# Kernel optimization log

Hardware: AMD Instinct MI355X
Metric: run time of the kernel (lower is better)

Reference implementation:

```python
import jax, jax.numpy as jnp
import numpy as np
from jax import lax

NUM_INPUT = 4
NUM_OUTPUT = 1
NUM_U = 10
N = NUM_U // NUM_OUTPUT          # MPC horizon
BATCH = 1024
NINEQ_U = 2 * NUM_U              # input box constraints
NINEQ_X = 2 * NUM_INPUT * N      # soft state constraints
NZ = NUM_U                       # control decision variable dim
NE = NINEQ_X                     # slack variable dim
NW = NZ + NE                     # combined QP variable w = [z; e]
IPM_ITERS = 20                   # fixed-iteration primal-dual interior point
SIGMA = 0.1                      # centering parameter
REG = 1e-8                       # KKT regularization


def setup_inputs():
    key = jax.random.key(0)
    ks = jax.random.split(key, 6)
    x = 0.5 * jax.random.normal(ks[0], (BATCH, NUM_INPUT), dtype=jnp.float32)
    # equality constraint pins z0 = u0; keep inside the |z| <= 0.5 box so QP is feasible
    u0 = (jax.random.uniform(ks[1], (BATCH, NUM_OUTPUT), dtype=jnp.float32) - 0.5) * 0.8
    Q_sqrt = jax.random.uniform(ks[2], (NUM_INPUT, NUM_INPUT), dtype=jnp.float32)
    R_sqrt = jax.random.uniform(ks[3], (NUM_OUTPUT, NUM_OUTPUT), dtype=jnp.float32)
    # scale A so that A^N stays bounded (torch init rand() would blow up at N=10)
    A_dyn = 0.3 * jax.random.uniform(ks[4], (NUM_INPUT, NUM_INPUT), dtype=jnp.float32)
    B_dyn = jax.random.uniform(ks[5], (NUM_INPUT, NUM_OUTPUT), dtype=jnp.float32)
    return {"x": x, "u0": u0, "Q_sqrt": Q_sqrt, "R_sqrt": R_sqrt,
            "A_dyn": A_dyn, "B_dyn": B_dyn}


def _build_mpc_blocks(A, B):
    # A_hat = [A; A^2; ...; A^N],  B_hat = lower block-Toeplitz of A^k B
    Apows = [A]
    for _ in range(1, N):
        Apows.append(Apows[-1] @ A)
    A_hat = jnp.concatenate(Apows, axis=0)                 # (N*n, n)
    T = [B]
    for _ in range(1, N):
        T.append(A @ T[-1])
    T = jnp.stack(T)                                        # (N, n, m), T[k] = A^k B
    i = jnp.arange(N)
    diff = i[:, None] - i[None, :]
    blocks = jnp.where((diff >= 0)[:, :, None, None],
                       T[jnp.clip(diff, 0, N - 1)], 0.0)    # (N, N, n, m)
    B_hat = blocks.transpose(0, 2, 1, 3).reshape(N * NUM_INPUT, N * NUM_OUTPUT)
    return A_hat, B_hat


def _max_step(v, dv):
    # largest alpha keeping v + alpha*dv > 0 (per batch row)
    ratio = jnp.where(dv < -1e-12, -v / jnp.minimum(dv, -1e-12), 1e8)
    return jnp.min(ratio, axis=-1, keepdims=True)


def _qp_solve(H, q, G, h, Aeq, beq):
    # min 0.5 w^T H w + q^T w  s.t. G w <= h, Aeq w = beq
    # H, G, Aeq shared; q, h, beq batched. Infeasible-start primal-dual IPM.
    b, nw = q.shape
    mI = G.shape[0]
    ne = Aeq.shape[0]
    w = jnp.zeros((b, nw), q.dtype)
    nu = jnp.zeros((b, ne), q.dtype)
    s = jnp.maximum(h, 1.0)
    lam = jnp.ones((b, mI), q.dtype)
    I_nw = jnp.eye(nw, dtype=q.dtype)
    I_ne = jnp.eye(ne, dtype=q.dtype)

    def step(carry, _):
        w, s, lam, nu = carry
        Gw = w @ G.T
        r_dual = w @ H + q + lam @ G + nu @ Aeq            # (b, nw)
        r_prim = Gw + s - h                                # (b, mI)
        r_eq = w @ Aeq.T - beq                             # (b, ne)
        mu = SIGMA * jnp.sum(s * lam, axis=-1, keepdims=True) / mI
        d = lam / s
        tmp = (mu - lam * s + lam * r_prim) / s
        rw = -(r_dual + tmp @ G)
        rn = -r_eq
        # Schur complement in w: M = H + G^T diag(lam/s) G
        M = H[None] + (G.T[None, :, :] * d[:, None, :]) @ G + REG * I_nw
        AeqT = jnp.broadcast_to(Aeq.T[None], (b, nw, ne))
        AeqB = jnp.broadcast_to(Aeq[None], (b, ne, nw))
        corner = jnp.broadcast_to((-REG * I_ne)[None], (b, ne, ne))
        K = jnp.concatenate([jnp.concatenate([M, AeqT], axis=2),
                             jnp.concatenate([AeqB, corner], axis=2)], axis=1)
        rhs = jnp.concatenate([rw, rn], axis=1)
        sol = jnp.linalg.solve(K, rhs[..., None])[..., 0]
        dw, dnu = sol[:, :nw], sol[:, nw:]
        ds = -(dw @ G.T) - r_prim
        dlam = (mu - lam * s - lam * ds) / s
        alpha = 0.99 * jnp.minimum(1.0, jnp.minimum(_max_step(s, ds),
                                                    _max_step(lam, dlam)))
        return (w + alpha * dw, s + alpha * ds,
                lam + alpha * dlam, nu + alpha * dnu), None

    (w, s, lam, nu), _ = lax.scan(step, (w, s, lam, nu), None, length=IPM_ITERS)
    return w


def _forward(x, u0, Q_sqrt, R_sqrt, A_dyn, B_dyn):
    b = x.shape[0]
    dt = x.dtype
    x0 = x.reshape(b, -1)
    A_hat, B_hat = _build_mpc_blocks(A_dyn, B_dyn)
    Q = Q_sqrt @ Q_sqrt.T
    R = R_sqrt @ R_sqrt.T
    Q_diag = jnp.kron(jnp.eye(N, dtype=dt), Q)   # block-diag(Q,...,Q,P) with P = Q
    R_diag = jnp.kron(jnp.eye(N, dtype=dt), R)
    Q_hat = B_hat.T @ (Q_diag @ B_hat) + R_diag  # (nz, nz)
    A_x0 = x0 @ A_hat.T                           # (b, n*N)
    p = 2.0 * A_x0 @ (Q_diag @ B_hat)             # (b, nz)
    G1 = jnp.concatenate([jnp.eye(NZ, dtype=dt), -jnp.eye(NZ, dtype=dt)], axis=0)
    G2 = jnp.concatenate([B_hat, -B_hat], axis=0)
    h1 = 0.5 * jnp.ones((b, NINEQ_U), dt)
    h21 = 4.0 * jnp.ones((b, NUM_INPUT * N), dt) - A_x0
    h22 = 4.0 * jnp.ones((b, NUM_INPUT * N), dt) + A_x0
    h2 = jnp.concatenate([h21, h22], axis=1)
    E = jnp.eye(NE, dtype=dt)                     # E_sqrt = I so E = I
    # combined QP over w = [z; e]:
    #   min z^T Q_hat z + p^T z + e^T E e
    #   s.t. G1 z <= h1, G2 z - e <= h2, -e <= 0, F z = f
    # (sum_squares(sqrtm(Q_hat) z) == z^T Q_hat z, so sqrtm cancels exactly)
    H = 2.0 * jnp.block([[Q_hat, jnp.zeros((NZ, NE), dt)],
                         [jnp.zeros((NE, NZ), dt), E]])
    q = jnp.concatenate([p, jnp.zeros((b, NE), dt)], axis=1)
    Ie = jnp.eye(NE, dtype=dt)
    G_all = jnp.concatenate([
        jnp.concatenate([G1, jnp.zeros((NINEQ_U, NE), dt)], axis=1),
        jnp.concatenate([G2, -Ie], axis=1),
        jnp.concatenate([jnp.zeros((NE, NZ), dt), -Ie], axis=1)], axis=0)
    h_all = jnp.concatenate([h1, h2, jnp.zeros((b, NE), dt)], axis=1)
    F = jnp.zeros((1, NW), dt).at[0, 0].set(1.0)  # F z = f with F = e_0^T (padded over e)
    beq = u0.reshape(b, -1)
    w = _qp_solve(H, q, G_all, h_all, F, beq)
    u_opt = w[:, :NZ]
    e_opt = w[:, NZ:]
    a = jnp.sum((u_opt @ Q_hat) * u_opt + p * u_opt, axis=1)
    bterm = jnp.sum((A_x0 @ Q_diag) * A_x0, axis=1)
    c = jnp.sum((x0 @ Q) * x0, axis=1)
    dterm = jnp.sum((e_opt @ E) * e_opt, axis=1)
    cost_opt = (a + bterm + c + dterm)[:, None]
    u0_opt = u_opt[:, 0]   # weight vector is e_0
    return cost_opt, u0_opt


def reference(x, u0, Q_sqrt, R_sqrt, A_dyn, B_dyn):
    return _forward(x, u0, Q_sqrt, R_sqrt, A_dyn, B_dyn)
```

## Files before the change

kernel.cpp:

```cpp
#include <hip/hip_runtime.h>

#define BATCH 1024
#define ITERS 20
#define SIGMA_C 0.1f
#define REG_C 1e-8f

typedef float f2 __attribute__((ext_vector_type(2)));

__device__ __forceinline__ float frcp(float x) { return __builtin_amdgcn_rcpf(x); }
__device__ __forceinline__ float readlane_f(float v, int l) {
    return __int_as_float(__builtin_amdgcn_readlane(__float_as_int(v), l));
}
__device__ __forceinline__ f2 mkf2(float a, float b) { f2 r; r.x = a; r.y = b; return r; }
__device__ __forceinline__ f2 fma2(f2 a, f2 b, f2 c) { return a * b + c; }

#define DPPF(v, ctrl) \
    __int_as_float(__builtin_amdgcn_update_dpp(0, __float_as_int(v), ctrl, 0xf, 0xf, true))

__device__ __forceinline__ float wave_sum(float v) {
    v += DPPF(v, 0xB1);
    v += DPPF(v, 0x4E);
    v += DPPF(v, 0x141);
    v += DPPF(v, 0x140);
    v += __shfl_xor(v, 16);
    v += __shfl_xor(v, 32);
    return v;
}

#define RED4_DPP(ctrl) do { \
    p0 += DPPF(p0, ctrl); \
    p1 += DPPF(p1, ctrl); \
    p2 += DPPF(p2, ctrl); \
    q = fmaxf(q, DPPF(q, ctrl)); \
} while (0)

__global__ __launch_bounds__(64, 1) void ipm_kernel(
    const float* __restrict__ x, const float* __restrict__ u0p,
    const float* __restrict__ Qs, const float* __restrict__ Rs,
    const float* __restrict__ Ad, const float* __restrict__ Bd,
    float* __restrict__ out)
{
    const int item = blockIdx.x;
    const int lane = threadIdx.x;

    __shared__ __align__(16) float BLc[10 * 40];
    __shared__ __align__(16) float QBc[10 * 40];
    __shared__ __align__(16) float yL4[40];
    __shared__ __align__(16) float QhL[10 * 12];
    __shared__ __align__(16) float SL[10 * 12];
    __shared__ __align__(16) float cg[80];
    __shared__ float duL[20], ltL[20];
    __shared__ float axL[40];
    __shared__ float pvL[10], wL[10];
    __shared__ float QL[16];
    __shared__ float TL[40];
    __shared__ float AhL[160];

    const int r2 = (lane >> 2) & 3, c2 = lane & 3;
    const int r4 = lane & 3;

    if (lane < 16) {
        float acc = 0.f;
        #pragma unroll
        for (int k = 0; k < 4; ++k) acc += Qs[r2 * 4 + k] * Qs[c2 * 4 + k];
        QL[lane] = acc;
    }

    float acol[4];
    #pragma unroll
    for (int k = 0; k < 4; ++k) acol[k] = Ad[k * 4 + c2];
    float cur = Ad[r2 * 4 + c2];
    if (lane < 16) AhL[r2 * 4 + c2] = cur;
    #pragma unroll
    for (int i = 1; i < 10; ++i) {
        float nx = 0.f;
        #pragma unroll
        for (int k = 0; k < 4; ++k) nx += __shfl(cur, r2 * 4 + k) * acol[k];
        cur = nx;
        if (lane < 16) AhL[(4 * i + r2) * 4 + c2] = cur;
    }

    float arow[4];
    #pragma unroll
    for (int k = 0; k < 4; ++k) arow[k] = Ad[r4 * 4 + k];
    float tc = Bd[r4];
    if (lane < 4) TL[r4] = tc;
    #pragma unroll
    for (int i = 1; i < 10; ++i) {
        float nt = 0.f;
        #pragma unroll
        for (int k = 0; k < 4; ++k) nt += arow[k] * __shfl(tc, k);
        tc = nt;
        if (lane < 4) TL[i * 4 + r4] = nt;
    }
    __syncthreads();

    const int kk40 = (lane < 40) ? lane : 39;
    const int ib = lane >> 2;
    float b[10];
    #pragma unroll
    for (int j = 0; j < 10; ++j) {
        int dd = ib - j;
        int dc = dd < 0 ? 0 : (dd > 9 ? 9 : dd);
        float v = TL[dc * 4 + r4];
        b[j] = (dd >= 0 && lane < 40) ? v : 0.f;
    }

    const float xv0 = x[item * 4 + 0], xv1 = x[item * 4 + 1];
    const float xv2 = x[item * 4 + 2], xv3 = x[item * 4 + 3];
    const float ax = AhL[kk40 * 4 + 0] * xv0 + AhL[kk40 * 4 + 1] * xv1 +
                     AhL[kk40 * 4 + 2] * xv2 + AhL[kk40 * 4 + 3] * xv3;
    if (lane < 40) axL[lane] = ax;

    const int gbase = lane & ~3;
    float yv = 0.f;
    #pragma unroll
    for (int rp_ = 0; rp_ < 4; ++rp_) yv += QL[r4 * 4 + rp_] * __shfl(ax, gbase + rp_);
    if (lane < 40) yL4[lane] = yv;
    #pragma unroll
    for (int cc = 0; cc < 10; ++cc) {
        float acc = 0.f;
        #pragma unroll
        for (int rp_ = 0; rp_ < 4; ++rp_) acc += QL[r4 * 4 + rp_] * __shfl(b[cc], gbase + rp_);
        if (lane < 40) QBc[cc * 40 + lane] = acc;
    }
    if (lane < 40) {
        #pragma unroll
        for (int j = 0; j < 10; ++j) BLc[j * 40 + lane] = b[j];
    }
    __syncthreads();

    if (lane < 10) {
        const float4* br = reinterpret_cast<const float4*>(&BLc[lane * 40]);
        const float4* yy = reinterpret_cast<const float4*>(yL4);
        float acc = 0.f;
        #pragma unroll
        for (int i = 0; i < 10; ++i) {
            const float4 a_ = br[i], b_ = yy[i];
            acc += a_.x * b_.x + a_.y * b_.y + a_.z * b_.z + a_.w * b_.w;
        }
        pvL[lane] = 2.f * acc;
    }
    const float R2v = Rs[0] * Rs[0];
    #pragma unroll
    for (int p = 0; p < 2; ++p) {
        const int t = lane + 64 * p;
        if (t < 100) {
            const int aa = t / 10, bb = t - aa * 10;
            const float4* ba = reinterpret_cast<const float4*>(&BLc[aa * 40]);
            const float4* qb = reinterpret_cast<const float4*>(&QBc[bb * 40]);
            float acc = (aa == bb) ? R2v : 0.f;
            #pragma unroll
            for (int i = 0; i < 10; ++i) {
                const float4 a_ = ba[i], b_ = qb[i];
                acc += a_.x * b_.x + a_.y * b_.y + a_.z * b_.z + a_.w * b_.w;
            }
            QhL[aa * 12 + bb] = acc;
        }
    }
    __syncthreads();

    const int t1 = 2 * lane;
    const int srow = t1 / 10, sc1 = t1 - srow * 10, sc2 = sc1 + 1;
    const int rr = lane - 50;
    f2 tA[20], tB[20];
    float qh_a = 0.f, qh_b = 0.f;
    bool diagA = false, diagB = false;
    int drow = 0;
    if (lane < 50) {
        const float4* br = reinterpret_cast<const float4*>(&BLc[srow * 40]);
        const float4* b1 = reinterpret_cast<const float4*>(&BLc[sc1 * 40]);
        const float4* b2 = reinterpret_cast<const float4*>(&BLc[sc2 * 40]);
        #pragma unroll
        for (int i = 0; i < 10; ++i) {
            const float4 r_ = br[i], u_ = b1[i], v_ = b2[i];
            tA[2*i]   = mkf2(r_.x * u_.x, r_.y * u_.y);
            tA[2*i+1] = mkf2(r_.z * u_.z, r_.w * u_.w);
            tB[2*i]   = mkf2(r_.x * v_.x, r_.y * v_.y);
            tB[2*i+1] = mkf2(r_.z * v_.z, r_.w * v_.w);
        }
        qh_a = 2.f * QhL[srow * 12 + sc1];
        qh_b = 2.f * QhL[srow * 12 + sc2];
        diagA = (srow == sc1); diagB = (srow == sc2);
        drow = srow;
    } else if (lane < 60) {
        const float4* br = reinterpret_cast<const float4*>(&BLc[rr * 40]);
        #pragma unroll
        for (int i = 0; i < 10; ++i) {
            const float4 r_ = br[i];
            tA[2*i]   = mkf2(r_.x, r_.y);
            tA[2*i+1] = mkf2(r_.z, r_.w);
        }
        #pragma unroll
        for (int c = 0; c < 5; ++c)
            tB[c] = mkf2(QhL[rr * 12 + 2*c], QhL[rr * 12 + 2*c + 1]);
        qh_a = pvL[rr];
    }
    __syncthreads();

    float s_B = fmaxf(4.f - ax, 1.f), s_C = fmaxf(4.f + ax, 1.f);
    float s_D = 1.f, s_E = 1.f, s_U = 1.f;
    float l_B = 1.f, l_C = 1.f, l_D = 1.f, l_E = 1.f, l_U = 1.f;
    float w2a = 0.f, w2b = 0.f;
    float w1[10];
    #pragma unroll
    for (int r = 0; r < 10; ++r) w1[r] = 0.f;
    float w1own = 0.f, nu = 0.f;
    const float uu0 = u0p[item];
    const bool a40 = lane < 40, a20 = lane < 20;
    const int jown = (lane < 10) ? lane : lane - 10;
    const float sgnU = (lane < 10) ? 1.f : -1.f;

    float mu;
    {
        float part = a40 ? (s_B * l_B + s_C * l_C + s_D * l_D + s_E * l_E) : 0.f;
        if (a20) part += s_U * l_U;
        mu = SIGMA_C * wave_sum(part) * (1.f / 180.f);
    }

    for (int it = 0; it < ITERS; ++it) {
        const float rs_B = frcp(s_B), rs_C = frcp(s_C), rs_D = frcp(s_D),
                    rs_E = frcp(s_E), rs_U = frcp(s_U);
        const float rl_B = frcp(l_B), rl_C = frcp(l_C), rl_D = frcp(l_D),
                    rl_E = frcp(l_E), rl_U = frcp(l_U);
        const float d_B = l_B * rs_B, d_C = l_C * rs_C, d_D = l_D * rs_D,
                    d_E = l_E * rs_E, d_U = l_U * rs_U;

        f2 bu = mkf2(0.f, 0.f);
        #pragma unroll
        for (int j = 0; j < 5; ++j)
            bu = fma2(mkf2(b[2*j], b[2*j+1]), mkf2(w1[2*j], w1[2*j+1]), bu);
        const float Bu = bu.x + bu.y;

        const float rp_B = Bu - w2a + s_B - (4.f - ax);
        const float rp_C = -Bu - w2b + s_C - (4.f + ax);
        const float rp_D = -w2a + s_D;
        const float rp_E = -w2b + s_E;
        const float rp_U = sgnU * w1own + s_U - 0.5f;

        const float tm_B = (mu - l_B * s_B + l_B * rp_B) * rs_B;
        const float tm_C = (mu - l_C * s_C + l_C * rp_C) * rs_C;
        const float tm_D = (mu - l_D * s_D + l_D * rp_D) * rs_D;
        const float tm_E = (mu - l_E * s_E + l_E * rp_E) * rs_E;
        const float tm_U = (mu - l_U * s_U + l_U * rp_U) * rs_U;
        const float lt_B = l_B + tm_B, lt_C = l_C + tm_C, lt_D = l_D + tm_D,
                    lt_E = l_E + tm_E;

        const float D22a = 2.f + d_B + d_D + REG_C, D22b = 2.f + d_C + d_E + REG_C;
        const float rda = frcp(D22a), rdb = frcp(D22b);
        const float rw2a = -2.f * w2a + lt_B + lt_D;
        const float rw2b = -2.f * w2b + lt_C + lt_E;
        const float coeff = (d_B + d_C) - d_B * d_B * rda - d_C * d_C * rdb;
        const float gvc = (d_B * rw2a * rda - d_C * rw2b * rdb) - (lt_B - lt_C);

        if (a40) { cg[lane] = coeff; cg[40 + lane] = gvc; }
        if (a20) { duL[lane] = d_U; ltL[lane] = l_U + tm_U; }
        __syncthreads();

        float4 cf4[10];
        {
            const float4* cp = reinterpret_cast<const float4*>(cg + ((lane >= 50) ? 40 : 0));
            #pragma unroll
            for (int i = 0; i < 10; ++i) cf4[i] = cp[i];
        }
        if (lane < 50) {
            f2 aA0 = mkf2(0.f, 0.f), aA1 = mkf2(0.f, 0.f);
            f2 aB0 = mkf2(0.f, 0.f), aB1 = mkf2(0.f, 0.f);
            #pragma unroll
            for (int i = 0; i < 10; ++i) {
                const f2 cl = mkf2(cf4[i].x, cf4[i].y);
                const f2 ch = mkf2(cf4[i].z, cf4[i].w);
                aA0 = fma2(tA[2*i], cl, aA0); aA1 = fma2(tA[2*i+1], ch, aA1);
                aB0 = fma2(tB[2*i], cl, aB0); aB1 = fma2(tB[2*i+1], ch, aB1);
            }
            float vA = ((aA0.x + aA0.y) + (aA1.x + aA1.y)) + qh_a;
            float vB = ((aB0.x + aB0.y) + (aB1.x + aB1.y)) + qh_b;
            if (diagA || diagB) {
                const float dd = duL[drow] + duL[10 + drow] + REG_C;
                if (diagA) vA += dd; else vB += dd;
            }
            *reinterpret_cast<float2*>(&SL[srow * 12 + sc1]) = make_float2(vA, vB);
        } else if (lane < 60) {
            f2 a0 = mkf2(0.f, 0.f), a1 = mkf2(0.f, 0.f);
            #pragma unroll
            for (int i = 0; i < 10; ++i) {
                const f2 cl = mkf2(cf4[i].x, cf4[i].y);
                const f2 ch = mkf2(cf4[i].z, cf4[i].w);
                a0 = fma2(tA[2*i], cl, a0); a1 = fma2(tA[2*i+1], ch, a1);
            }
            const float acc = (a0.x + a0.y) + (a1.x + a1.y);
            f2 qa = mkf2(0.f, 0.f);
            #pragma unroll
            for (int c = 0; c < 5; ++c)
                qa = fma2(tB[c], mkf2(w1[2*c], w1[2*c+1]), qa);
            const float qw = qa.x + qa.y;
            SL[rr * 12 + 10] =
                acc - (2.f * qw + qh_a + ltL[rr] - ltL[10 + rr] + ((rr == 0) ? nu : 0.f));
        }
        __syncthreads();

        float row[11], rBv;
        if (lane < 10) {
            const float4* s4 = reinterpret_cast<const float4*>(&SL[lane * 12]);
            const float4 q0 = s4[0], q1 = s4[1], q2 = s4[2];
            row[0] = q0.x; row[1] = q0.y; row[2] = q0.z; row[3] = q0.w;
            row[4] = q1.x; row[5] = q1.y; row[6] = q1.z; row[7] = q1.w;
            row[8] = q2.x; row[9] = q2.y; row[10] = q2.z;
        } else {
            #pragma unroll
            for (int c = 0; c < 11; ++c) row[c] = 0.f;
        }
        rBv = (lane == 0) ? 1.f : 0.f;

        #pragma unroll
        for (int kc = 0; kc < 9; ++kc) {
            float pk[11];
            #pragma unroll
            for (int c = kc; c < 11; ++c) pk[c] = readlane_f(row[c], kc);
            const float pB = readlane_f(rBv, kc);
            const float rpiv = frcp(pk[kc]);
            const float f = (lane > kc) ? row[kc] * rpiv : 0.f;
            #pragma unroll
            for (int c = kc + 1; c < 11; ++c) row[c] -= f * pk[c];
            rBv -= f * pB;
        }

        float rd[10];
        #pragma unroll
        for (int r = 0; r < 10; ++r) rd[r] = frcp(row[r]);

        float dwAv[10], dwBv[10], ownA = 0.f, ownB = 0.f;
        #pragma unroll
        for (int r = 9; r >= 0; --r) {
            const float bA = readlane_f(row[10] * rd[r], r);
            const float bB = readlane_f(rBv * rd[r], r);
            dwAv[r] = bA; dwBv[r] = bB;
            if (jown == r) { ownA = bA; ownB = bB; }
            const float m_ = (lane < r) ? 1.f : 0.f;
            row[10] -= m_ * row[r] * bA;
            rBv     -= m_ * row[r] * bB;
        }

        const float rn = -(w1[0] - uu0);
        const float nu_d = (dwAv[0] - rn) * frcp(dwBv[0] + REG_C);
        float dw1[10];
        #pragma unroll
        for (int r = 0; r < 10; ++r) dw1[r] = dwAv[r] - nu_d * dwBv[r];
        const float dOwn = ownA - nu_d * ownB;

        f2 bd = mkf2(0.f, 0.f);
        #pragma unroll
        for (int j = 0; j < 5; ++j)
            bd = fma2(mkf2(b[2*j], b[2*j+1]), mkf2(dw1[2*j], dw1[2*j+1]), bd);
        const float Bdw = bd.x + bd.y;

        const float dw2a = (rw2a + d_B * Bdw) * rda;
        const float dw2b = (rw2b - d_C * Bdw) * rdb;

        const float ds_B = -(Bdw - dw2a) - rp_B;
        const float ds_C = (Bdw + dw2b) - rp_C;
        const float ds_D = dw2a - rp_D;
        const float ds_E = dw2b - rp_E;
        const float ds_U = -sgnU * dOwn - rp_U;
        const float dl_B = (mu - l_B * s_B - l_B * ds_B) * rs_B;
        const float dl_C = (mu - l_C * s_C - l_C * ds_C) * rs_C;
        const float dl_D = (mu - l_D * s_D - l_D * ds_D) * rs_D;
        const float dl_E = (mu - l_E * s_E - l_E * ds_E) * rs_E;
        const float dl_U = (mu - l_U * s_U - l_U * ds_U) * rs_U;

        float q = 0.f, p0 = 0.f, p1 = 0.f, p2 = 0.f;
        if (a40) {
            q = fmaxf(q, (ds_B < -1e-12f) ? -ds_B * rs_B : 0.f);
            q = fmaxf(q, (ds_C < -1e-12f) ? -ds_C * rs_C : 0.f);
            q = fmaxf(q, (ds_D < -1e-12f) ? -ds_D * rs_D : 0.f);
            q = fmaxf(q, (ds_E < -1e-12f) ? -ds_E * rs_E : 0.f);
            q = fmaxf(q, (dl_B < -1e-12f) ? -dl_B * rl_B : 0.f);
            q = fmaxf(q, (dl_C < -1e-12f) ? -dl_C * rl_C : 0.f);
            q = fmaxf(q, (dl_D < -1e-12f) ? -dl_D * rl_D : 0.f);
            q = fmaxf(q, (dl_E < -1e-12f) ? -dl_E * rl_E : 0.f);
            p0 = s_B * l_B + s_C * l_C + s_D * l_D + s_E * l_E;
            p1 = (s_B * dl_B + l_B * ds_B) + (s_C * dl_C + l_C * ds_C) +
                 (s_D * dl_D + l_D * ds_D) + (s_E * dl_E + l_E * ds_E);
            p2 = ds_B * dl_B + ds_C * dl_C + ds_D * dl_D + ds_E * dl_E;
        }
        if (a20) {
            q = fmaxf(q, (ds_U < -1e-12f) ? -ds_U * rs_U : 0.f);
            q = fmaxf(q, (dl_U < -1e-12f) ? -dl_U * rl_U : 0.f);
            p0 += s_U * l_U;
            p1 += s_U * dl_U + l_U * ds_U;
            p2 += ds_U * dl_U;
        }
        RED4_DPP(0xB1);
        RED4_DPP(0x4E);
        RED4_DPP(0x141);
        RED4_DPP(0x140);
        p0 += __shfl_xor(p0, 16); p1 += __shfl_xor(p1, 16); p2 += __shfl_xor(p2, 16);
        q = fmaxf(q, __shfl_xor(q, 16));
        p0 += __shfl_xor(p0, 32); p1 += __shfl_xor(p1, 32); p2 += __shfl_xor(p2, 32);
        q = fmaxf(q, __shfl_xor(q, 32));

        const float alpha = 0.99f * ((q > 1.f) ? frcp(q) : 1.f);
        mu = SIGMA_C * (p0 + alpha * (p1 + alpha * p2)) * (1.f / 180.f);

        s_B += alpha * ds_B; s_C += alpha * ds_C; s_D += alpha * ds_D;
        s_E += alpha * ds_E; s_U += alpha * ds_U;
        l_B += alpha * dl_B; l_C += alpha * dl_C; l_D += alpha * dl_D;
        l_E += alpha * dl_E; l_U += alpha * dl_U;
        w2a += alpha * dw2a; w2b += alpha * dw2b;
        #pragma unroll
        for (int r = 0; r < 10; ++r) w1[r] += alpha * dw1[r];
        w1own += alpha * dOwn;
        nu += alpha * nu_d;
    }

    if (lane == 0) {
        #pragma unroll
        for (int r = 0; r < 10; ++r) wL[r] = w1[r];
    }
    __syncthreads();
    float part = a40 ? (w2a * w2a + w2b * w2b) : 0.f;
    for (int idx = lane; idx < 100; idx += 64) {
        const int r = idx / 10, c = idx - r * 10;
        part += wL[r] * QhL[r * 12 + c] * wL[c];
    }
    if (lane < 10) part += pvL[lane] * wL[lane];
    for (int idx = lane; idx < 160; idx += 64) {
        const int i2 = idx >> 4, rc = idx & 15, rr2 = rc >> 2, cc2 = rc & 3;
        part += axL[i2 * 4 + rr2] * QL[rc] * axL[i2 * 4 + cc2];
    }
    if (lane == 0) {
        float ct = 0.f;
        #pragma unroll
        for (int r = 0; r < 4; ++r) {
            const float xr = (r == 0 ? xv0 : r == 1 ? xv1 : r == 2 ? xv2 : xv3);
            #pragma unroll
            for (int c = 0; c < 4; ++c) {
                const float xc = (c == 0 ? xv0 : c == 1 ? xv1 : c == 2 ? xv2 : xv3);
                ct += xr * QL[r * 4 + c] * xc;
            }
        }
        part += ct;
    }
    const float cost = wave_sum(part);
    if (lane == 0) {
        out[item] = cost;
        out[BATCH + item] = w1[0];
    }
}

extern "C" void kernel_launch(void* const* d_in, const int* in_sizes, int n_in,
                              void* d_out, int out_size, void* d_ws, size_t ws_size,
                              hipStream_t stream) {
    const float* x  = (const float*)d_in[0];
    const float* u0 = (const float*)d_in[1];
    const float* Qs = (const float*)d_in[2];
    const float* Rs = (const float*)d_in[3];
    const float* Ad = (const float*)d_in[4];
    const float* Bd = (const float*)d_in[5];
    float* outp = (float*)d_out;
    ipm_kernel<<<dim3(BATCH), dim3(64), 0, stream>>>(x, u0, Qs, Rs, Ad, Bd, outp);
}
```

Measured before the change: 99.50 us.

## Replace block barriers with wave barriers and keep RHS in registers

Because the block is a single 64-lane wavefront, the per-iteration __syncthreads calls become wave barriers with a compiler memory fence. Lane roles are remapped so the 10 RHS lanes are lanes 0-9, which lets the RHS value stay in a register instead of being written to shared memory and read back. The p0 complementarity sum is computed and reduced early, overlapping with the Schur-complement build, so it drops out of the end-of-iteration DPP reduction. The change relies on LDS ordering within one wave and on the wave_barrier-plus-asm fence being sufficient.

```diff
diff --git a/kernel.cpp b/kernel.cpp
--- a/kernel.cpp
+++ b/kernel.cpp
@@ -13,6 +13,8 @@
 }
 __device__ __forceinline__ f2 mkf2(float a, float b) { f2 r; r.x = a; r.y = b; return r; }
 __device__ __forceinline__ f2 fma2(f2 a, f2 b, f2 c) { return a * b + c; }
+
+#define WFENCE() do { __builtin_amdgcn_wave_barrier(); asm volatile("" ::: "memory"); } while (0)
 
 #define DPPF(v, ctrl) \
     __int_as_float(__builtin_amdgcn_update_dpp(0, __float_as_int(v), ctrl, 0xf, 0xf, true))
@@ -27,8 +29,7 @@
     return v;
 }
 
-#define RED4_DPP(ctrl) do { \
-    p0 += DPPF(p0, ctrl); \
+#define RED3_DPP(ctrl) do { \
     p1 += DPPF(p1, ctrl); \
     p2 += DPPF(p2, ctrl); \
     q = fmaxf(q, DPPF(q, ctrl)); \
@@ -160,14 +161,14 @@
     }
     __syncthreads();
 
-    const int t1 = 2 * lane;
+    const bool rLane = (lane < 10);
+    const bool sLane = (lane >= 10 && lane < 60);
+    const int t1 = sLane ? 2 * (lane - 10) : 0;
     const int srow = t1 / 10, sc1 = t1 - srow * 10, sc2 = sc1 + 1;
-    const int rr = lane - 50;
     f2 tA[20], tB[20];
     float qh_a = 0.f, qh_b = 0.f;
     bool diagA = false, diagB = false;
-    int drow = 0;
-    if (lane < 50) {
+    if (sLane) {
         const float4* br = reinterpret_cast<const float4*>(&BLc[srow * 40]);
         const float4* b1 = reinterpret_cast<const float4*>(&BLc[sc1 * 40]);
         const float4* b2 = reinterpret_cast<const float4*>(&BLc[sc2 * 40]);
@@ -182,9 +183,8 @@
         qh_a = 2.f * QhL[srow * 12 + sc1];
         qh_b = 2.f * QhL[srow * 12 + sc2];
         diagA = (srow == sc1); diagB = (srow == sc2);
-        drow = srow;
-    } else if (lane < 60) {
-        const float4* br = reinterpret_cast<const float4*>(&BLc[rr * 40]);
+    } else if (rLane) {
+        const float4* br = reinterpret_cast<const float4*>(&BLc[lane * 40]);
         #pragma unroll
         for (int i = 0; i < 10; ++i) {
             const float4 r_ = br[i];
@@ -193,8 +193,8 @@
         }
         #pragma unroll
         for (int c = 0; c < 5; ++c)
-            tB[c] = mkf2(QhL[rr * 12 + 2*c], QhL[rr * 12 + 2*c + 1]);
-        qh_a = pvL[rr];
+            tB[c] = mkf2(QhL[lane * 12 + 2*c], QhL[lane * 12 + 2*c + 1]);
+        qh_a = pvL[lane];
     }
     __syncthreads();
 
@@ -255,15 +255,21 @@
 
         if (a40) { cg[lane] = coeff; cg[40 + lane] = gvc; }
         if (a20) { duL[lane] = d_U; ltL[lane] = l_U + tm_U; }
-        __syncthreads();
+        WFENCE();
 
         float4 cf4[10];
         {
-            const float4* cp = reinterpret_cast<const float4*>(cg + ((lane >= 50) ? 40 : 0));
+            const float4* cp = reinterpret_cast<const float4*>(cg + (rLane ? 40 : 0));
             #pragma unroll
             for (int i = 0; i < 10; ++i) cf4[i] = cp[i];
         }
-        if (lane < 50) {
+
+        float p0 = a40 ? (s_B * l_B + s_C * l_C + s_D * l_D + s_E * l_E) : 0.f;
+        if (a20) p0 += s_U * l_U;
+        p0 = wave_sum(p0);
+
+        float rhs_loc = 0.f;
+        if (sLane) {
             f2 aA0 = mkf2(0.f, 0.f), aA1 = mkf2(0.f, 0.f);
             f2 aB0 = mkf2(0.f, 0.f), aB1 = mkf2(0.f, 0.f);
             #pragma unroll
@@ -276,11 +282,11 @@
             float vA = ((aA0.x + aA0.y) + (aA1.x + aA1.y)) + qh_a;
             float vB = ((aB0.x + aB0.y) + (aB1.x + aB1.y)) + qh_b;
             if (diagA || diagB) {
-                const float dd = duL[drow] + duL[10 + drow] + REG_C;
+                const float dd = duL[srow] + duL[10 + srow] + REG_C;
                 if (diagA) vA += dd; else vB += dd;
             }
             *reinterpret_cast<float2*>(&SL[srow * 12 + sc1]) = make_float2(vA, vB);
-        } else if (lane < 60) {
+        } else if (rLane) {
             f2 a0 = mkf2(0.f, 0.f), a1 = mkf2(0.f, 0.f);
             #pragma unroll
             for (int i = 0; i < 10; ++i) {
@@ -294,22 +300,24 @@
             for (int c = 0; c < 5; ++c)
                 qa = fma2(tB[c], mkf2(w1[2*c], w1[2*c+1]), qa);
             const float qw = qa.x + qa.y;
-            SL[rr * 12 + 10] =
-                acc - (2.f * qw + qh_a + ltL[rr] - ltL[10 + rr] + ((rr == 0) ? nu : 0.f));
-        }
-        __syncthreads();
+            rhs_loc = acc - (2.f * qw + qh_a + ltL[lane] - ltL[10 + lane] +
+                             ((lane == 0) ? nu : 0.f));
+        }
+        WFENCE();
 
         float row[11], rBv;
-        if (lane < 10) {
+        if (rLane) {
             const float4* s4 = reinterpret_cast<const float4*>(&SL[lane * 12]);
             const float4 q0 = s4[0], q1 = s4[1], q2 = s4[2];
             row[0] = q0.x; row[1] = q0.y; row[2] = q0.z; row[3] = q0.w;
             row[4] = q1.x; row[5] = q1.y; row[6] = q1.z; row[7] = q1.w;
-            row[8] = q2.x; row[9] = q2.y; row[10] = q2.z;
+            row[8] = q2.x; row[9] = q2.y;
+            (void)q2;
         } else {
             #pragma unroll
-            for (int c = 0; c < 11; ++c) row[c] = 0.f;
-        }
+            for (int c = 0; c < 10; ++c) row[c] = 0.f;
+        }
+        row[10] = rhs_loc;
         rBv = (lane == 0) ? 1.f : 0.f;
 
         #pragma unroll
@@ -368,7 +376,7 @@
         const float dl_E = (mu - l_E * s_E - l_E * ds_E) * rs_E;
         const float dl_U = (mu - l_U * s_U - l_U * ds_U) * rs_U;
 
-        float q = 0.f, p0 = 0.f, p1 = 0.f, p2 = 0.f;
+        float q = 0.f, p1 = 0.f, p2 = 0.f;
         if (a40) {
             q = fmaxf(q, (ds_B < -1e-12f) ? -ds_B * rs_B : 0.f);
             q = fmaxf(q, (ds_C < -1e-12f) ? -ds_C * rs_C : 0.f);
@@ -378,7 +386,6 @@
             q = fmaxf(q, (dl_C < -1e-12f) ? -dl_C * rl_C : 0.f);
             q = fmaxf(q, (dl_D < -1e-12f) ? -dl_D * rl_D : 0.f);
             q = fmaxf(q, (dl_E < -1e-12f) ? -dl_E * rl_E : 0.f);
-            p0 = s_B * l_B + s_C * l_C + s_D * l_D + s_E * l_E;
             p1 = (s_B * dl_B + l_B * ds_B) + (s_C * dl_C + l_C * ds_C) +
                  (s_D * dl_D + l_D * ds_D) + (s_E * dl_E + l_E * ds_E);
             p2 = ds_B * dl_B + ds_C * dl_C + ds_D * dl_D + ds_E * dl_E;
@@ -386,17 +393,16 @@
         if (a20) {
             q = fmaxf(q, (ds_U < -1e-12f) ? -ds_U * rs_U : 0.f);
             q = fmaxf(q, (dl_U < -1e-12f) ? -dl_U * rl_U : 0.f);
-            p0 += s_U * l_U;
             p1 += s_U * dl_U + l_U * ds_U;
             p2 += ds_U * dl_U;
         }
-        RED4_DPP(0xB1);
-        RED4_DPP(0x4E);
-        RED4_DPP(0x141);
-        RED4_DPP(0x140);
-        p0 += __shfl_xor(p0, 16); p1 += __shfl_xor(p1, 16); p2 += __shfl_xor(p2, 16);
+        RED3_DPP(0xB1);
+        RED3_DPP(0x4E);
+        RED3_DPP(0x141);
+        RED3_DPP(0x140);
+        p1 += __shfl_xor(p1, 16); p2 += __shfl_xor(p2, 16);
         q = fmaxf(q, __shfl_xor(q, 16));
-        p0 += __shfl_xor(p0, 32); p1 += __shfl_xor(p1, 32); p2 += __shfl_xor(p2, 32);
+        p1 += __shfl_xor(p1, 32); p2 += __shfl_xor(p2, 32);
         q = fmaxf(q, __shfl_xor(q, 32));
 
         const float alpha = 0.99f * ((q > 1.f) ? frcp(q) : 1.f);
@@ -411,6 +417,7 @@
         for (int r = 0; r < 10; ++r) w1[r] += alpha * dw1[r];
         w1own += alpha * dOwn;
         nu += alpha * nu_d;
+        WFENCE();
     }
 
     if (lane == 0) {
```

Measured after the change: 99.72 us. About the same (+0.2%).
